# Kernel optimization log

Measured on AMD Instinct MI355X. Metric: run time of the kernel, lower is better.

## Reference

```python
import jax, jax.numpy as jnp
import numpy as np

B, T, V, D, H, L = 256, 256, 128, 384, 6, 6
HS = D // H  # 64
FF = 4 * D


def _ln(x, g, b):
    m = jnp.mean(x, axis=-1, keepdims=True)
    v = jnp.var(x, axis=-1, keepdims=True)
    return (x - m) / jnp.sqrt(v + 1e-5) * g + b


def setup_inputs() -> dict:
    key = jax.random.key(0)
    ks = jax.random.split(key, 16)
    s = lambda k, sh: jax.random.normal(k, sh, dtype=jnp.float32) * 0.02
    return {
        "idx": jax.random.randint(ks[0], (B, T), 0, V),
        "tok_emb": s(ks[1], (V, D)),
        "pos_emb": s(ks[2], (T, D)),
        "Wq": s(ks[3], (L, H, D, HS)),
        "Wk": s(ks[4], (L, H, D, HS)),
        "Wv": s(ks[5], (L, H, D, HS)),
        "Wproj": s(ks[6], (L, D, D)),
        "bproj": jnp.zeros((L, D), jnp.float32),
        "ln1_g": jnp.ones((L, D), jnp.float32),
        "ln1_b": jnp.zeros((L, D), jnp.float32),
        "ln2_g": jnp.ones((L, D), jnp.float32),
        "ln2_b": jnp.zeros((L, D), jnp.float32),
        "W1": s(ks[7], (L, D, FF)),
        "b1": jnp.zeros((L, FF), jnp.float32),
        "W2": s(ks[8], (L, FF, D)),
        "b2": jnp.zeros((L, D), jnp.float32),
        "lnf_g": jnp.ones((D,), jnp.float32),
        "lnf_b": jnp.zeros((D,), jnp.float32),
        "Wlm": s(ks[9], (D, V)),
        "blm": jnp.zeros((V,), jnp.float32),
    }


def reference(idx, tok_emb, pos_emb, Wq, Wk, Wv, Wproj, bproj,
              ln1_g, ln1_b, ln2_g, ln2_b, W1, b1, W2, b2,
              lnf_g, lnf_b, Wlm, blm):
    Bv, Tv = idx.shape
    x = tok_emb[idx] + pos_emb[:Tv]  # [B,T,D]
    mask = jnp.tril(jnp.ones((Tv, Tv), dtype=bool))
    scale = HS ** -0.5
    for l in range(L):
        xn = _ln(x, ln1_g[l], ln1_b[l])
        q = jnp.einsum('btd,hdk->bhtk', xn, Wq[l])
        k = jnp.einsum('btd,hdk->bhtk', xn, Wk[l])
        v = jnp.einsum('btd,hdk->bhtk', xn, Wv[l])
        wei = jnp.einsum('bhtk,bhsk->bhts', q, k) * scale  # [B,H,T,T]
        wei = jnp.where(mask, wei, -jnp.inf)
        wei = jax.nn.softmax(wei, axis=-1)
        o = jnp.einsum('bhts,bhsk->bhtk', wei, v)
        o = o.transpose(0, 2, 1, 3).reshape(Bv, Tv, D)  # concat heads
        x = x + o @ Wproj[l] + bproj[l]
        xn = _ln(x, ln2_g[l], ln2_b[l])
        x = x + jax.nn.relu(xn @ W1[l] + b1[l]) @ W2[l] + b2[l]
    x = _ln(x, lnf_g, lnf_b)
    return x @ Wlm + blm  # logits [B,T,V]
```

## Files before the change

### kernel.cpp

```cpp
#include <hip/hip_runtime.h>
#include <stdint.h>

typedef unsigned short u16;
typedef __attribute__((ext_vector_type(8))) short short8;
typedef __attribute__((ext_vector_type(4))) float floatx4;

#define BB 256
#define TT 256
#define VOC 128
#define DD 384
#define HH 6
#define LLAY 6
#define HS 64
#define FFF 1536
#define BT (BB*TT)

__device__ __forceinline__ float b2f(u16 u) {
  union { float f; uint32_t i; } x; x.i = ((uint32_t)u) << 16; return x.f;
}
__device__ __forceinline__ u16 f2b(float f) {
  union { float f; uint32_t i; } x; x.f = f;
  uint32_t r = x.i + 0x7fffu + ((x.i >> 16) & 1u);
  return (u16)(r >> 16);
}
__device__ __forceinline__ float ldf(const void* p, size_t i, int bf) {
  return bf ? b2f(((const u16*)p)[i]) : ((const float*)p)[i];
}
__device__ __forceinline__ int get_bf(const u16* probe) {
  return probe[0] == 0x3F80;
}

__device__ __forceinline__ void gl2lds16(const u16* g, u16* l) {
  __builtin_amdgcn_global_load_lds(
      (const __attribute__((address_space(1))) unsigned int*)g,
      (__attribute__((address_space(3))) unsigned int*)l, 16, 0, 0);
}

__global__ __launch_bounds__(256) void k_repack_qkv(
    const void* __restrict__ Wq, const void* __restrict__ Wk,
    const void* __restrict__ Wv, u16* __restrict__ out,
    const void* __restrict__ g1, const void* __restrict__ b1n,
    float* __restrict__ u, float* __restrict__ v, const u16* probe) {
  __shared__ float t[32][33];
  int bf = get_bf(probe);
  int z = blockIdx.z;
  int h = z % 6, ls = z / 6, sel = ls % 3, l = ls / 3;
  const void* W = sel == 0 ? Wq : (sel == 1 ? Wk : Wv);
  int c0 = blockIdx.x * 32;
  int r0 = blockIdx.y * 32;
  int tx = threadIdx.x & 31, ty = threadIdx.x >> 5;
#pragma unroll
  for (int i = 0; i < 32; i += 8)
    t[ty + i][tx] = ldf(W, (((size_t)(l * 6 + h)) * 384 + r0 + ty + i) * 64 + c0 + tx, bf);
  __syncthreads();
  float gv = ldf(g1, (size_t)l * 384 + r0 + tx, bf);
  float bv = ldf(b1n, (size_t)l * 384 + r0 + tx, bf);
#pragma unroll
  for (int i = 0; i < 32; i += 8) {
    float w = t[tx][ty + i];
    int n = sel * 384 + h * 64 + c0 + ty + i;
    out[((size_t)l * 1152 + n) * 384 + r0 + tx] = f2b(w * gv);
    float pu = w * gv, pv = w * bv;
#pragma unroll
    for (int m = 1; m < 32; m <<= 1) { pu += __shfl_xor(pu, m); pv += __shfl_xor(pv, m); }
    if (tx == 0) {
      atomicAdd(&u[(size_t)l * 1152 + n], pu);
      atomicAdd(&v[(size_t)l * 1152 + n], pv);
    }
  }
}

__global__ __launch_bounds__(256) void k_transpose(
    const void* __restrict__ in, u16* __restrict__ out, int R, int C,
    const u16* probe) {
  __shared__ float t[32][33];
  int bf = get_bf(probe);
  int c0 = blockIdx.x * 32, r0 = blockIdx.y * 32, l = blockIdx.z;
  int tx = threadIdx.x & 31, ty = threadIdx.x >> 5;
  size_t base = (size_t)l * R * C;
#pragma unroll
  for (int i = 0; i < 32; i += 8)
    t[ty + i][tx] = ldf(in, base + (size_t)(r0 + ty + i) * C + c0 + tx, bf);
  __syncthreads();
#pragma unroll
  for (int i = 0; i < 32; i += 8)
    out[base + (size_t)(c0 + ty + i) * R + r0 + tx] = f2b(t[tx][ty + i]);
}

__global__ __launch_bounds__(256) void k_transpose_ln(
    const void* __restrict__ in, u16* __restrict__ out, int R, int C,
    const void* __restrict__ g, const void* __restrict__ b,
    float* __restrict__ u, float* __restrict__ v, const u16* probe) {
  __shared__ float t[32][33];
  int bf = get_bf(probe);
  int c0 = blockIdx.x * 32, r0 = blockIdx.y * 32, l = blockIdx.z;
  int tx = threadIdx.x & 31, ty = threadIdx.x >> 5;
  size_t base = (size_t)l * R * C;
#pragma unroll
  for (int i = 0; i < 32; i += 8)
    t[ty + i][tx] = ldf(in, base + (size_t)(r0 + ty + i) * C + c0 + tx, bf);
  __syncthreads();
  float gv = ldf(g, (size_t)l * R + r0 + tx, bf);
  float bv = ldf(b, (size_t)l * R + r0 + tx, bf);
#pragma unroll
  for (int i = 0; i < 32; i += 8) {
    float w = t[tx][ty + i];
    out[base + (size_t)(c0 + ty + i) * R + r0 + tx] = f2b(w * gv);
    float pu = w * gv, pv = w * bv;
#pragma unroll
    for (int m = 1; m < 32; m <<= 1) { pu += __shfl_xor(pu, m); pv += __shfl_xor(pv, m); }
    if (tx == 0) {
      atomicAdd(&u[(size_t)l * C + c0 + ty + i], pu);
      atomicAdd(&v[(size_t)l * C + c0 + ty + i], pv);
    }
  }
}

__global__ __launch_bounds__(256) void k_embed(
    const int* __restrict__ idx, const void* __restrict__ tok,
    const void* __restrict__ pos, u16* __restrict__ X,
    float* __restrict__ stp, const u16* probe) {
  int bf = get_bf(probe);
  int gw = (blockIdx.x * 256 + threadIdx.x) >> 6;
  int lane = threadIdx.x & 63;
  int nw = (gridDim.x * 256) >> 6;
  for (int row = gw; row < BT; row += nw) {
    int v = idx[row];
    size_t tb = (size_t)v * DD, pb = (size_t)(row & 255) * DD;
    u16* xr = X + (size_t)row * DD;
    float s = 0.f, ss = 0.f;
#pragma unroll
    for (int i = 0; i < 6; ++i) {
      int d = i * 64 + lane;
      float x = ldf(tok, tb + d, bf) + ldf(pos, pb + d, bf);
      u16 xb = f2b(x);
      xr[d] = xb;
      float v2 = b2f(xb);
      s += v2; ss += v2 * v2;
    }
#pragma unroll
    for (int m = 1; m < 64; m <<= 1) { s += __shfl_xor(s, m); ss += __shfl_xor(ss, m); }
    if (lane < 6) {
      float2 pr;
      pr.x = (lane == 0) ? s : 0.f;
      pr.y = (lane == 0) ? ss : 0.f;
      *(float2*)(stp + (size_t)row * 12 + lane * 2) = pr;
    }
  }
}

template <int EPI>
__global__ __launch_bounds__(512) void k_gemm(
    const u16* __restrict__ A, const u16* __restrict__ Bt,
    const void* __restrict__ bias, int boff, u16* __restrict__ Xb,
    u16* __restrict__ C, float* __restrict__ Cf, int N, int K,
    const float* __restrict__ u, const float* __restrict__ v,
    float* __restrict__ stp, const u16* probe) {
  __shared__ u16 As[256 * 64];
  __shared__ u16 Bs[128 * 64];
  __shared__ float stl[256][2];
  int tid = threadIdx.x, lane = tid & 63, wave = tid >> 6;
  int m0 = blockIdx.x * 256, n0 = blockIdx.y * 128;

  if (EPI != 2) {
    if (tid < 256) {
      const float* p = stp + (size_t)(m0 + tid) * 12;
      float s = 0.f, ss = 0.f;
#pragma unroll
      for (int k2 = 0; k2 < 6; ++k2) { s += p[2 * k2]; ss += p[2 * k2 + 1]; }
      float mean = s * (1.f / DD);
      float var = ss * (1.f / DD) - mean * mean;
      stl[tid][0] = mean;
      stl[tid][1] = rsqrtf(var + 1e-5f);
    }
  }

  int srow = tid >> 3;
  int skg = ((tid & 7) ^ (srow & 7)) * 8;
  const u16* gA = A + (size_t)(m0 + srow) * K + skg;
  const u16* gB = Bt + (size_t)(n0 + srow) * K + skg;
  u16* lA = As + wave * 512;
  u16* lB = Bs + wave * 512;
  int wy = wave >> 1, wx = wave & 1;
  int lr = lane & 15, quad = lane >> 4;
  int sx = lr & 7;
  floatx4 acc[4][4];
#pragma unroll
  for (int i = 0; i < 4; ++i)
#pragma unroll
    for (int j = 0; j < 4; ++j) acc[i][j] = (floatx4){0.f, 0.f, 0.f, 0.f};

  const u16* Abase = As + (size_t)(wy * 64 + lr) * 64;
  const u16* Bbase = Bs + (size_t)(wx * 64 + lr) * 64;

  int nk = K >> 6;
  for (int bk = 0; bk < nk; ++bk) {
    __syncthreads();
#pragma unroll
    for (int c = 0; c < 4; ++c)
      gl2lds16(gA + (size_t)(c * 64) * K, lA + c * 4096);
#pragma unroll
    for (int c = 0; c < 2; ++c)
      gl2lds16(gB + (size_t)(c * 64) * K, lB + c * 4096);
    gA += 64; gB += 64;
    __syncthreads();
#pragma unroll
    for (int half = 0; half < 2; ++half) {
      int ko = ((quad + half * 4) ^ sx) * 8;
      short8 af[4], bfr[4];
#pragma unroll
      for (int i = 0; i < 4; ++i) af[i] = *(const short8*)(Abase + i * 1024 + ko);
#pragma unroll
      for (int j = 0; j < 4; ++j) bfr[j] = *(const short8*)(Bbase + j * 1024 + ko);
#pragma unroll
      for (int i = 0; i < 4; ++i)
#pragma unroll
        for (int j = 0; j < 4; ++j)
          acc[i][j] = __builtin_amdgcn_mfma_f32_16x16x32_bf16(af[i], bfr[j], acc[i][j], 0, 0, 0);
    }
  }

  if (EPI == 2) {
    int bfl = get_bf(probe);
    float bv2[4];
#pragma unroll
    for (int j = 0; j < 4; ++j)
      bv2[j] = ldf(bias, boff + n0 + wx * 64 + j * 16 + lr, bfl);
    int slot = blockIdx.y * 2 + wx;
#pragma unroll
    for (int i = 0; i < 4; ++i) {
      int mrow = m0 + wy * 64 + i * 16 + quad * 4;
#pragma unroll
      for (int r = 0; r < 4; ++r) {
        int grow = mrow + r;
        float s = 0.f, ss = 0.f;
#pragma unroll
        for (int j = 0; j < 4; ++j) {
          int n = n0 + wx * 64 + j * 16 + lr;
          size_t off = (size_t)grow * N + n;
          u16 val = f2b(b2f(Xb[off]) + acc[i][j][r] + bv2[j]);
          Xb[off] = val;
          float yr = b2f(val);
          s += yr; ss += yr * yr;
        }
#pragma unroll
        for (int m = 1; m < 16; m <<= 1) { s += __shfl_xor(s, m); ss += __shfl_xor(ss, m); }
        if (lr == 0) {
          float2 pr; pr.x = s; pr.y = ss;
          *(float2*)(stp + ((size_t)grow * 6 + slot) * 2) = pr;
        }
      }
    }
  } else {
    int bfl = (EPI == 1 || EPI == 3) ? get_bf(probe) : 1;
    float un[4], vn[4], bv[4], sc[4];
    size_t sb[4]; int nc[4];
#pragma unroll
    for (int j = 0; j < 4; ++j) {
      int n = n0 + wx * 64 + j * 16 + lr;
      un[j] = u[n]; vn[j] = v[n];
      bv[j] = (EPI == 4) ? 0.f : ldf(bias, boff + n, bfl);
      sc[j] = 1.f;
      if (EPI == 4) {
        int sel = n >= 768 ? 2 : (n >= 384 ? 1 : 0);
        int hh = (n - sel * 384) >> 6;
        sb[j] = (size_t)sel * boff * 384 + (size_t)hh * boff * 64;
        nc[j] = n & 63;
        if (sel == 0) sc[j] = 0.125f;
      }
    }
#pragma unroll
    for (int i = 0; i < 4; ++i) {
      int lrow0 = wy * 64 + i * 16 + quad * 4;
#pragma unroll
      for (int r = 0; r < 4; ++r) {
        int lrow = lrow0 + r;
        int grow = m0 + lrow;
        float mu = stl[lrow][0], rs = stl[lrow][1];
#pragma unroll
        for (int j = 0; j < 4; ++j) {
          int n = n0 + wx * 64 + j * 16 + lr;
          float y = rs * (acc[i][j][r] - mu * un[j]) + vn[j];
          if (EPI == 1) C[(size_t)grow * N + n] = f2b(fmaxf(y + bv[j], 0.f));
          else if (EPI == 3) {
            if (bfl) C[(size_t)grow * N + n] = f2b(y + bv[j]);
            else Cf[(size_t)grow * N + n] = y + bv[j];
          } else {
            C[sb[j] + (size_t)grow * 64 + nc[j]] = f2b(y * sc[j]);
          }
        }
      }
    }
  }
}

__global__ __launch_bounds__(512, 6) void k_attn(
    const u16* __restrict__ Q, const u16* __restrict__ K,
    const u16* __restrict__ V, u16* __restrict__ O, int TB) {
  __shared__ u16 Vt[64 * 264];
  __shared__ u16 P[8][16 * 72];
  int h = blockIdx.x;
  int b = blockIdx.y;
  int tid = threadIdx.x, lane = tid & 63, wave = tid >> 6;
  int lr = lane & 15, quad = lane >> 4;
  size_t hbase = (size_t)h * TB;
  const u16* Vb = V + (hbase + b * TT) * 64;
  const u16* Kb = K + (hbase + b * TT) * 64;
  const u16* Qb = Q + (hbase + b * TT) * 64;

  {
    int rp = tid & 127, oc2 = tid >> 7;
    const u16* v0 = Vb + (size_t)(2 * rp) * 64 + oc2 * 16;
    short8 a0 = *(const short8*)(v0);
    short8 a1 = *(const short8*)(v0 + 8);
    short8 b0 = *(const short8*)(v0 + 64);
    short8 b1 = *(const short8*)(v0 + 72);
#pragma unroll
    for (int e = 0; e < 8; ++e) {
      int d0 = oc2 * 16 + e, d1 = d0 + 8;
      uint32_t p0 = (uint32_t)(u16)a0[e] | ((uint32_t)(u16)b0[e] << 16);
      uint32_t p1 = (uint32_t)(u16)a1[e] | ((uint32_t)(u16)b1[e] << 16);
      *(uint32_t*)&Vt[d0 * 264 + 2 * rp] = p0;
      *(uint32_t*)&Vt[d1 * 264 + 2 * rp] = p1;
    }
  }
  __syncthreads();

  u16* Pw = P[wave];
  const u16* Pr = Pw + lr * 72 + quad * 8;

#pragma unroll
  for (int tt = 0; tt < 2; ++tt) {
    int t = wave * 2 + tt;
    int r0 = t * 16;
    const u16* qrow = Qb + (size_t)(r0 + lr) * 64 + quad * 8;
    short8 qf0 = *(const short8*)(qrow);
    short8 qf1 = *(const short8*)(qrow + 32);
    int nk = (t >> 2) + 1;

    float ls[4];
    floatx4 oacc[4];
#pragma unroll
    for (int r = 0; r < 4; ++r) ls[r] = 0.f;
#pragma unroll
    for (int j2 = 0; j2 < 4; ++j2) oacc[j2] = (floatx4){0.f, 0.f, 0.f, 0.f};

    for (int ks = 0; ks < nk; ++ks) {
      floatx4 s[4];
#pragma unroll
      for (int cc = 0; cc < 4; ++cc) s[cc] = (floatx4){0.f, 0.f, 0.f, 0.f};
      const u16* kbase = Kb + (size_t)(ks * 64 + lr) * 64 + quad * 8;
#pragma unroll
      for (int cc = 0; cc < 4; ++cc) {
        const u16* kr = kbase + cc * 16 * 64;
        short8 kf;
        kf = *(const short8*)(kr);      s[cc] = __builtin_amdgcn_mfma_f32_16x16x32_bf16(qf0, kf, s[cc], 0, 0, 0);
        kf = *(const short8*)(kr + 32); s[cc] = __builtin_amdgcn_mfma_f32_16x16x32_bf16(qf1, kf, s[cc], 0, 0, 0);
      }

      if (ks == nk - 1) {
#pragma unroll
        for (int r = 0; r < 4; ++r) {
          int rowt = r0 + quad * 4 + r;
#pragma unroll
          for (int cc = 0; cc < 4; ++cc) {
            int c = ks * 64 + cc * 16 + lr;
            float e = (c > rowt) ? 0.f : __expf(s[cc][r]);
            ls[r] += e;
            Pw[(quad * 4 + r) * 72 + cc * 16 + lr] = f2b(e);
          }
        }
      } else {
#pragma unroll
        for (int r = 0; r < 4; ++r)
#pragma unroll
          for (int cc = 0; cc < 4; ++cc) {
            float e = __expf(s[cc][r]);
            ls[r] += e;
            Pw[(quad * 4 + r) * 72 + cc * 16 + lr] = f2b(e);
          }
      }
      asm volatile("s_waitcnt lgkmcnt(0)" ::: "memory");
#pragma unroll
      for (int h2 = 0; h2 < 2; ++h2) {
        short8 pf = *(const short8*)(Pr + h2 * 32);
#pragma unroll
        for (int j2 = 0; j2 < 4; ++j2) {
          short8 vf = *(const short8*)(Vt + (j2 * 16 + lr) * 264 + ks * 64 + h2 * 32 + quad * 8);
          oacc[j2] = __builtin_amdgcn_mfma_f32_16x16x32_bf16(pf, vf, oacc[j2], 0, 0, 0);
        }
      }
    }

#pragma unroll
    for (int r = 0; r < 4; ++r) {
#pragma unroll
      for (int mm = 1; mm < 16; mm <<= 1) ls[r] += __shfl_xor(ls[r], mm);
      ls[r] = 1.f / ls[r];
    }

    asm volatile("s_waitcnt lgkmcnt(0)" ::: "memory");
#pragma unroll
    for (int j2 = 0; j2 < 4; ++j2)
#pragma unroll
      for (int r = 0; r < 4; ++r)
        Pw[(quad * 4 + r) * 72 + j2 * 16 + lr] = f2b(oacc[j2][r] * ls[r]);
    asm volatile("s_waitcnt lgkmcnt(0)" ::: "memory");
#pragma unroll
    for (int p = 0; p < 2; ++p) {
      int idx = p * 64 + lane;
      int row = idx >> 3, cg = idx & 7;
      short8 o8 = *(const short8*)(Pw + row * 72 + cg * 8);
      *(short8*)(O + (size_t)(b * TT + r0 + row) * DD + h * 64 + cg * 8) = o8;
    }
    asm volatile("s_waitcnt lgkmcnt(0) vmcnt(0)" ::: "memory");
  }
}

extern "C" void kernel_launch(void* const* d_in, const int* in_sizes, int n_in,
                              void* d_out, int out_size, void* d_ws, size_t ws_size,
                              hipStream_t stream) {
  const int* idx   = (const int*)d_in[0];
  const void* tok  = d_in[1];
  const void* pos  = d_in[2];
  const void* Wq   = d_in[3];
  const void* Wk   = d_in[4];
  const void* Wv   = d_in[5];
  const void* Wproj= d_in[6];
  const void* bproj= d_in[7];
  const void* ln1g = d_in[8];
  const void* ln1b = d_in[9];
  const void* ln2g = d_in[10];
  const void* ln2b = d_in[11];
  const void* W1   = d_in[12];
  const void* b1   = d_in[13];
  const void* W2   = d_in[14];
  const void* b2   = d_in[15];
  const void* lnfg = d_in[16];
  const void* lnfb = d_in[17];
  const void* Wlm  = d_in[18];
  const void* blm  = d_in[19];
  const u16* probe = (const u16*)d_in[8];

  char* ws = (char*)d_ws;
  u16* X  = (u16*)ws;
  u16* XA = (u16*)(ws + 50331648);
  char* wb = ws + 100663296;
  u16* Wqkv_t  = (u16*)wb;
  u16* Wproj_t = (u16*)(wb + 5308416);
  u16* W1_t    = (u16*)(wb + 7077888);
  u16* W2_t    = (u16*)(wb + 14155776);
  u16* Wlm_t   = (u16*)(wb + 21233664);
  char* uvb = wb + 21331968;
  float* u_qkv = (float*)uvb;
  float* v_qkv = (float*)(uvb + 27648);
  float* u_fc1 = (float*)(uvb + 55296);
  float* v_fc1 = (float*)(uvb + 92160);
  float* u_lm  = (float*)(uvb + 129024);
  float* v_lm  = (float*)(uvb + 129536);
  float* stp   = (float*)(uvb + 130048 + 524288);
  const size_t fixed = 100663296 + 21331968 + 130048 + 524288 + 3145728;
  u16* S  = (u16*)(ws + fixed);

  size_t avail = ws_size > fixed ? ws_size - fixed : 0;
  int nA = 8, nM = 8;
  if ((size_t)BT * 1152 * 2 <= avail) nA = 1;
  else if ((size_t)(BT / 2) * 1152 * 2 <= avail) nA = 2;
  else if ((size_t)(BT / 4) * 1152 * 2 <= avail) nA = 4;
  if ((size_t)BT * 1536 * 2 <= avail) nM = 1;
  else if ((size_t)(BT / 2) * 1536 * 2 <= avail) nM = 2;
  else if ((size_t)(BT / 4) * 1536 * 2 <= avail) nM = 4;
  const int rowsA = BT / nA;
  const int rowsM = BT / nM;

  hipMemsetAsync(uvb, 0, 130048, stream);
  { dim3 g(2, 12, 108);
    k_repack_qkv<<<g, 256, 0, stream>>>(Wq, Wk, Wv, Wqkv_t, ln1g, ln1b,
                                        u_qkv, v_qkv, probe); }
  { dim3 g(12, 12, 6);   k_transpose<<<g, 256, 0, stream>>>(Wproj, Wproj_t, 384, 384, probe); }
  { dim3 g(48, 12, 6);
    k_transpose_ln<<<g, 256, 0, stream>>>(W1, W1_t, 384, 1536, ln2g, ln2b,
                                          u_fc1, v_fc1, probe); }
  { dim3 g(12, 48, 6);   k_transpose<<<g, 256, 0, stream>>>(W2, W2_t, 1536, 384, probe); }
  { dim3 g(4, 12, 1);
    k_transpose_ln<<<g, 256, 0, stream>>>(Wlm, Wlm_t, 384, 128, lnfg, lnfb,
                                          u_lm, v_lm, probe); }

  k_embed<<<2048, 256, 0, stream>>>(idx, tok, pos, X, stp, probe);

  for (int l = 0; l < LLAY; ++l) {
    for (int c = 0; c < nA; ++c) {
      const u16* A0c = X + (size_t)c * rowsA * DD;
      { dim3 g(rowsA / 256, 9);
        k_gemm<4><<<g, 512, 0, stream>>>(A0c, Wqkv_t + (size_t)l * 1152 * 384,
                                         nullptr, rowsA, nullptr, S, nullptr, 1152, 384,
                                         u_qkv + l * 1152, v_qkv + l * 1152,
                                         stp + (size_t)c * rowsA * 12, probe); }
      { dim3 g(HH, rowsA / TT);
        k_attn<<<g, 512, 0, stream>>>(S, S + (size_t)6 * rowsA * 64,
                                      S + (size_t)12 * rowsA * 64,
                                      XA + (size_t)c * rowsA * DD, rowsA); }
    }
    { dim3 g(256, 3);
      k_gemm<2><<<g, 512, 0, stream>>>(XA, Wproj_t + (size_t)l * 384 * 384,
                                       bproj, l * 384, X, nullptr, nullptr, 384, 384,
                                       nullptr, nullptr, stp, probe); }
    for (int c = 0; c < nM; ++c) {
      const u16* A0c = X + (size_t)c * rowsM * DD;
      { dim3 g(rowsM / 256, 12);
        k_gemm<1><<<g, 512, 0, stream>>>(A0c, W1_t + (size_t)l * 1536 * 384,
                                         b1, l * 1536, nullptr, S, nullptr, 1536, 384,
                                         u_fc1 + l * 1536, v_fc1 + l * 1536,
                                         stp + (size_t)c * rowsM * 12, probe); }
      { dim3 g(rowsM / 256, 3);
        k_gemm<2><<<g, 512, 0, stream>>>(S, W2_t + (size_t)l * 384 * 1536,
                                         b2, l * 384, X + (size_t)c * rowsM * DD,
                                         nullptr, nullptr, 384, 1536,
                                         nullptr, nullptr,
                                         stp + (size_t)c * rowsM * 12, probe); }
    }
  }
  { dim3 g(256, 1);
    k_gemm<3><<<g, 512, 0, stream>>>(X, Wlm_t, blm, 0, nullptr,
                                     (u16*)d_out, (float*)d_out, 128, 384,
                                     u_lm, v_lm, stp, probe); }
}
```

Before: 2.708 ms.

## Double-buffer GEMM LDS tiles and shrink blocks to 128x128 with 256 threads

Measured after the change: 3.471 ms. +28.2%, slower.

```diff
diff --git a/kernel.cpp b/kernel.cpp
--- a/kernel.cpp
+++ b/kernel.cpp
@@ -150,20 +150,20 @@
 }
 
 template <int EPI>
-__global__ __launch_bounds__(512) void k_gemm(
+__global__ __launch_bounds__(256) void k_gemm(
     const u16* __restrict__ A, const u16* __restrict__ Bt,
     const void* __restrict__ bias, int boff, u16* __restrict__ Xb,
     u16* __restrict__ C, float* __restrict__ Cf, int N, int K,
     const float* __restrict__ u, const float* __restrict__ v,
     float* __restrict__ stp, const u16* probe) {
-  __shared__ u16 As[256 * 64];
-  __shared__ u16 Bs[128 * 64];
-  __shared__ float stl[256][2];
+  __shared__ u16 As[2][128 * 64];
+  __shared__ u16 Bs[2][128 * 64];
+  __shared__ float stl[128][2];
   int tid = threadIdx.x, lane = tid & 63, wave = tid >> 6;
-  int m0 = blockIdx.x * 256, n0 = blockIdx.y * 128;
+  int m0 = blockIdx.x * 128, n0 = blockIdx.y * 128;
 
   if (EPI != 2) {
-    if (tid < 256) {
+    if (tid < 128) {
       const float* p = stp + (size_t)(m0 + tid) * 12;
       float s = 0.f, ss = 0.f;
 #pragma unroll
@@ -179,8 +179,6 @@
   int skg = ((tid & 7) ^ (srow & 7)) * 8;
   const u16* gA = A + (size_t)(m0 + srow) * K + skg;
   const u16* gB = Bt + (size_t)(n0 + srow) * K + skg;
-  u16* lA = As + wave * 512;
-  u16* lB = Bs + wave * 512;
   int wy = wave >> 1, wx = wave & 1;
   int lr = lane & 15, quad = lane >> 4;
   int sx = lr & 7;
@@ -190,20 +188,32 @@
 #pragma unroll
     for (int j = 0; j < 4; ++j) acc[i][j] = (floatx4){0.f, 0.f, 0.f, 0.f};
 
-  const u16* Abase = As + (size_t)(wy * 64 + lr) * 64;
-  const u16* Bbase = Bs + (size_t)(wx * 64 + lr) * 64;
-
   int nk = K >> 6;
+
+#pragma unroll
+  for (int c = 0; c < 4; ++c)
+    gl2lds16(gA + (size_t)(c * 32) * K, &As[0][wave * 512 + c * 2048]);
+#pragma unroll
+  for (int c = 0; c < 4; ++c)
+    gl2lds16(gB + (size_t)(c * 32) * K, &Bs[0][wave * 512 + c * 2048]);
+  gA += 64; gB += 64;
+
   for (int bk = 0; bk < nk; ++bk) {
+    asm volatile("s_waitcnt vmcnt(0)" ::: "memory");
     __syncthreads();
-#pragma unroll
-    for (int c = 0; c < 4; ++c)
-      gl2lds16(gA + (size_t)(c * 64) * K, lA + c * 4096);
-#pragma unroll
-    for (int c = 0; c < 2; ++c)
-      gl2lds16(gB + (size_t)(c * 64) * K, lB + c * 4096);
-    gA += 64; gB += 64;
-    __syncthreads();
+    if (bk + 1 < nk) {
+      int nb = (bk + 1) & 1;
+#pragma unroll
+      for (int c = 0; c < 4; ++c)
+        gl2lds16(gA + (size_t)(c * 32) * K, &As[nb][wave * 512 + c * 2048]);
+#pragma unroll
+      for (int c = 0; c < 4; ++c)
+        gl2lds16(gB + (size_t)(c * 32) * K, &Bs[nb][wave * 512 + c * 2048]);
+      gA += 64; gB += 64;
+    }
+    int cb = bk & 1;
+    const u16* Abase = &As[cb][(wy * 64 + lr) * 64];
+    const u16* Bbase = &Bs[cb][(wx * 64 + lr) * 64];
 #pragma unroll
     for (int half = 0; half < 2; ++half) {
       int ko = ((quad + half * 4) ^ sx) * 8;
@@ -491,8 +501,8 @@
   for (int l = 0; l < LLAY; ++l) {
     for (int c = 0; c < nA; ++c) {
       const u16* A0c = X + (size_t)c * rowsA * DD;
-      { dim3 g(rowsA / 256, 9);
-        k_gemm<4><<<g, 512, 0, stream>>>(A0c, Wqkv_t + (size_t)l * 1152 * 384,
+      { dim3 g(rowsA / 128, 9);
+        k_gemm<4><<<g, 256, 0, stream>>>(A0c, Wqkv_t + (size_t)l * 1152 * 384,
                                          nullptr, rowsA, nullptr, S, nullptr, 1152, 384,
                                          u_qkv + l * 1152, v_qkv + l * 1152,
                                          stp + (size_t)c * rowsA * 12, probe); }
@@ -501,27 +511,27 @@
                                       S + (size_t)12 * rowsA * 64,
                                       XA + (size_t)c * rowsA * DD, rowsA); }
     }
-    { dim3 g(256, 3);
-      k_gemm<2><<<g, 512, 0, stream>>>(XA, Wproj_t + (size_t)l * 384 * 384,
+    { dim3 g(BT / 128, 3);
+      k_gemm<2><<<g, 256, 0, stream>>>(XA, Wproj_t + (size_t)l * 384 * 384,
                                        bproj, l * 384, X, nullptr, nullptr, 384, 384,
                                        nullptr, nullptr, stp, probe); }
     for (int c = 0; c < nM; ++c) {
       const u16* A0c = X + (size_t)c * rowsM * DD;
-      { dim3 g(rowsM / 256, 12);
-        k_gemm<1><<<g, 512, 0, stream>>>(A0c, W1_t + (size_t)l * 1536 * 384,
+      { dim3 g(rowsM / 128, 12);
+        k_gemm<1><<<g, 256, 0, stream>>>(A0c, W1_t + (size_t)l * 1536 * 384,
                                          b1, l * 1536, nullptr, S, nullptr, 1536, 384,
                                          u_fc1 + l * 1536, v_fc1 + l * 1536,
                                          stp + (size_t)c * rowsM * 12, probe); }
-      { dim3 g(rowsM / 256, 3);
-        k_gemm<2><<<g, 512, 0, stream>>>(S, W2_t + (size_t)l * 384 * 1536,
+      { dim3 g(rowsM / 128, 3);
+        k_gemm<2><<<g, 256, 0, stream>>>(S, W2_t + (size_t)l * 384 * 1536,
                                          b2, l * 384, X + (size_t)c * rowsM * DD,
                                          nullptr, nullptr, 384, 1536,
                                          nullptr, nullptr,
                                          stp + (size_t)c * rowsM * 12, probe); }
     }
   }
-  { dim3 g(256, 1);
-    k_gemm<3><<<g, 512, 0, stream>>>(X, Wlm_t, blm, 0, nullptr,
+  { dim3 g(BT / 128, 1);
+    k_gemm<3><<<g, 256, 0, stream>>>(X, Wlm_t, blm, 0, nullptr,
                                      (u16*)d_out, (float*)d_out, 128, 384,
                                      u_lm, v_lm, stp, probe); }
 }
```

## Double-buffer GEMM LDS tiles with async global-to-LDS prefetch

Applied to the files above, without the earlier changes.

Measured after the change: 3.650 ms. 34.8% more time.

```diff
diff --git a/kernel.cpp b/kernel.cpp
--- a/kernel.cpp
+++ b/kernel.cpp
@@ -156,8 +156,8 @@
     u16* __restrict__ C, float* __restrict__ Cf, int N, int K,
     const float* __restrict__ u, const float* __restrict__ v,
     float* __restrict__ stp, const u16* probe) {
-  __shared__ u16 As[256 * 64];
-  __shared__ u16 Bs[128 * 64];
+  __shared__ u16 As[2][256 * 64];
+  __shared__ u16 Bs[2][128 * 64];
   __shared__ float stl[256][2];
   int tid = threadIdx.x, lane = tid & 63, wave = tid >> 6;
   int m0 = blockIdx.x * 256, n0 = blockIdx.y * 128;
@@ -173,14 +173,13 @@
       stl[tid][0] = mean;
       stl[tid][1] = rsqrtf(var + 1e-5f);
     }
+    asm volatile("s_waitcnt lgkmcnt(0)" ::: "memory");
   }
 
   int srow = tid >> 3;
   int skg = ((tid & 7) ^ (srow & 7)) * 8;
   const u16* gA = A + (size_t)(m0 + srow) * K + skg;
   const u16* gB = Bt + (size_t)(n0 + srow) * K + skg;
-  u16* lA = As + wave * 512;
-  u16* lB = Bs + wave * 512;
   int wy = wave >> 1, wx = wave & 1;
   int lr = lane & 15, quad = lane >> 4;
   int sx = lr & 7;
@@ -190,20 +189,32 @@
 #pragma unroll
     for (int j = 0; j < 4; ++j) acc[i][j] = (floatx4){0.f, 0.f, 0.f, 0.f};
 
-  const u16* Abase = As + (size_t)(wy * 64 + lr) * 64;
-  const u16* Bbase = Bs + (size_t)(wx * 64 + lr) * 64;
-
   int nk = K >> 6;
+
+#pragma unroll
+  for (int c = 0; c < 4; ++c)
+    gl2lds16(gA + (size_t)(c * 64) * K, &As[0][wave * 512 + c * 4096]);
+#pragma unroll
+  for (int c = 0; c < 2; ++c)
+    gl2lds16(gB + (size_t)(c * 64) * K, &Bs[0][wave * 512 + c * 4096]);
+  gA += 64; gB += 64;
+#pragma unroll
+  for (int c = 0; c < 4; ++c)
+    gl2lds16(gA + (size_t)(c * 64) * K, &As[1][wave * 512 + c * 4096]);
+#pragma unroll
+  for (int c = 0; c < 2; ++c)
+    gl2lds16(gB + (size_t)(c * 64) * K, &Bs[1][wave * 512 + c * 4096]);
+  gA += 64; gB += 64;
+
   for (int bk = 0; bk < nk; ++bk) {
-    __syncthreads();
-#pragma unroll
-    for (int c = 0; c < 4; ++c)
-      gl2lds16(gA + (size_t)(c * 64) * K, lA + c * 4096);
-#pragma unroll
-    for (int c = 0; c < 2; ++c)
-      gl2lds16(gB + (size_t)(c * 64) * K, lB + c * 4096);
-    gA += 64; gB += 64;
-    __syncthreads();
+    if (bk + 1 < nk) asm volatile("s_waitcnt vmcnt(6)" ::: "memory");
+    else             asm volatile("s_waitcnt vmcnt(0)" ::: "memory");
+    __builtin_amdgcn_s_barrier();
+    asm volatile("" ::: "memory");
+    int cb = bk & 1;
+    const u16* Abase = &As[cb][(wy * 64 + lr) * 64];
+    const u16* Bbase = &Bs[cb][(wx * 64 + lr) * 64];
+    __builtin_amdgcn_s_setprio(1);
 #pragma unroll
     for (int half = 0; half < 2; ++half) {
       int ko = ((quad + half * 4) ^ sx) * 8;
@@ -217,6 +228,20 @@
 #pragma unroll
         for (int j = 0; j < 4; ++j)
           acc[i][j] = __builtin_amdgcn_mfma_f32_16x16x32_bf16(af[i], bfr[j], acc[i][j], 0, 0, 0);
+    }
+    __builtin_amdgcn_s_setprio(0);
+    asm volatile("" ::: "memory");
+    __builtin_amdgcn_s_barrier();
+    asm volatile("" ::: "memory");
+    if (bk + 2 < nk) {
+      int nb = bk & 1;
+#pragma unroll
+      for (int c = 0; c < 4; ++c)
+        gl2lds16(gA + (size_t)(c * 64) * K, &As[nb][wave * 512 + c * 4096]);
+#pragma unroll
+      for (int c = 0; c < 2; ++c)
+        gl2lds16(gB + (size_t)(c * 64) * K, &Bs[nb][wave * 512 + c * 4096]);
+      gA += 64; gB += 64;
     }
   }
 
@@ -501,7 +526,7 @@
                                       S + (size_t)12 * rowsA * 64,
                                       XA + (size_t)c * rowsA * DD, rowsA); }
     }
-    { dim3 g(256, 3);
+    { dim3 g(BT / 256, 3);
       k_gemm<2><<<g, 512, 0, stream>>>(XA, Wproj_t + (size_t)l * 384 * 384,
                                        bproj, l * 384, X, nullptr, nullptr, 384, 384,
                                        nullptr, nullptr, stp, probe); }
@@ -520,7 +545,7 @@
                                          stp + (size_t)c * rowsM * 12, probe); }
     }
   }
-  { dim3 g(256, 1);
+  { dim3 g(BT / 256, 1);
     k_gemm<3><<<g, 512, 0, stream>>>(X, Wlm_t, blm, 0, nullptr,
                                      (u16*)d_out, (float*)d_out, 128, 384,
                                      u_lm, v_lm, stp, probe); }
```
